# Kernel tuning notes

Hardware: AMD Instinct MI355X
Metric: run time of the kernel (lower is better)

The kernel has to match this reference:

```python
import jax, jax.numpy as jnp
import numpy as np

N, C, G = 50000, 30, 1000   # cells, classes, genes
E = 800000                   # edges
OUT = 8                      # GATv2 out channels, heads=1


def setup_inputs() -> dict:
    key = jax.random.key(0)
    ks = jax.random.split(key, 12)
    X = jax.random.normal(ks[0], (N, G), dtype=jnp.float32)
    Mu = jax.random.normal(ks[1], (C, G), dtype=jnp.float32)
    Var = jax.random.uniform(ks[2], (C, G), dtype=jnp.float32) + 0.5  # strictly positive
    edge_index = jax.random.randint(ks[3], (2, E), 0, N, dtype=jnp.int64)
    # learned params
    W = 0.01 * jax.random.normal(ks[4], (N, C), dtype=jnp.float32)   # torch init zeros; small noise for nontrivial P
    S = jnp.ones((N, 1), dtype=jnp.float32)
    sc = 1.0 / np.sqrt(G)
    Wl = sc * jax.random.normal(ks[5], (OUT, G), dtype=jnp.float32)  # lin_l weight
    bl = jnp.zeros((OUT,), dtype=jnp.float32)
    Wr = sc * jax.random.normal(ks[6], (OUT, G), dtype=jnp.float32)  # lin_r weight
    br = jnp.zeros((OUT,), dtype=jnp.float32)
    att = jax.random.normal(ks[7], (OUT,), dtype=jnp.float32) / np.sqrt(OUT)
    return {"X": X, "Mu": Mu, "Var": Var, "edge_index": edge_index,
            "W": W, "S": S, "Wl": Wl, "bl": bl, "Wr": Wr, "br": br, "att": att}


def reference(X, Mu, Var, edge_index, W, S, Wl, bl, Wr, br, att):
    n = X.shape[0]
    P = jax.nn.softmax(W, axis=1)                       # [N,C]
    # Gaussian log-likelihood term. Expand (X - Mu*S)^2/Var summed over genes:
    invVar = 1.0 / Var                                  # [C,G]
    A = (X * X) @ invVar.T                              # [N,C]  sum X^2/Var
    B = X @ (Mu * invVar).T                             # [N,C]  sum X*Mu/Var
    D = jnp.sum(Mu * Mu * invVar, axis=1)               # [C]    sum Mu^2/Var
    Fmat = -0.5 * (A - 2.0 * S * B + (S * S) * D[None, :])  # [N,C]
    ll_prot = jnp.sum(P * Fmat) / n

    # GATv2 attention (heads=1, add_self_loops=False)
    x_l = X @ Wl.T + bl                                 # [N,8] source transform
    x_r = X @ Wr.T + br                                 # [N,8] target transform
    src, dst = edge_index[0], edge_index[1]
    m = jax.nn.leaky_relu(x_l[src] + x_r[dst], negative_slope=0.2)  # [E,8]
    e = m @ att                                         # [E]
    # edge-softmax grouped by destination node
    emax = jax.ops.segment_max(e, dst, num_segments=n)  # [N]
    e_exp = jnp.exp(e - emax[dst])                      # [E]
    denom = jax.ops.segment_sum(e_exp, dst, num_segments=n)  # [N]
    alpha = e_exp / (denom[dst] + 1e-16)                # [E]

    ce_space = -jnp.sum(P[src] * alpha[:, None] * jnp.log(P[dst] + 1e-8)) / n
    return ll_prot, ce_space, P
```

## Files before the change

### kernel.cpp

```cpp
#include <hip/hip_runtime.h>
#include <math.h>

#define N_CELLS 50000
#define C_CLS   30
#define G_GENES 1000
#define E_EDGES 800000
#define KPAD    1024

typedef __attribute__((ext_vector_type(8))) short bf16x8;
typedef __attribute__((ext_vector_type(4))) float f32x4;

__device__ __forceinline__ unsigned f2bf_u(float f) {
    unsigned u = __float_as_uint(f);
    return (u + 0x7fffu + ((u >> 16) & 1u)) >> 16;
}
__device__ __forceinline__ unsigned pack2(float lo, float hi) {
    return f2bf_u(lo) | (f2bf_u(hi) << 16);
}

__device__ __forceinline__ float lrelu02(float v) { return v > 0.f ? v : 0.2f * v; }

__global__ void prep_kernel(const float* __restrict__ Mu, const float* __restrict__ Var,
                            const float* __restrict__ Wl, const float* __restrict__ Wr,
                            unsigned short* __restrict__ CoefB, float* __restrict__ Dvec) {
    const int r = blockIdx.x;
    const int t = threadIdx.x;
    __shared__ float red[256];
    float dacc = 0.f;
    for (int g = t; g < KPAD; g += 256) {
        float v = 0.f;
        if (g < G_GENES) {
            if (r < 30) {
                float iv = 1.0f / Var[r * G_GENES + g];
                float mu = Mu[r * G_GENES + g];
                v = iv;
                dacc += mu * mu * iv;
            } else if (r >= 32) {
                int i = r - 32;
                if (i < 30)      v = Mu[i * G_GENES + g] / Var[i * G_GENES + g];
                else if (i < 38) v = Wl[(i - 30) * G_GENES + g];
                else if (i < 46) v = Wr[(i - 38) * G_GENES + g];
            }
        }
        CoefB[r * KPAD + g] = (unsigned short)f2bf_u(v);
    }
    if (r < 30) {
        red[t] = dacc;
        __syncthreads();
        for (int s = 128; s > 0; s >>= 1) {
            if (t < s) red[t] += red[t + s];
            __syncthreads();
        }
        if (t == 0) Dvec[r] = red[0];
    }
}

__global__ __launch_bounds__(256) void main_rows_kernel(
    const float* __restrict__ X, const float* __restrict__ W,
    const float* __restrict__ S, const float* __restrict__ bl,
    const float* __restrict__ br, const unsigned short* __restrict__ CoefB,
    const float* __restrict__ Dvec,
    float* __restrict__ out,
    float* __restrict__ logP, float* __restrict__ xl, float* __restrict__ xr)
{
    __shared__ __align__(16) char smem[30720];
    unsigned short* Xt  = (unsigned short*)smem;
    unsigned short* X2t = (unsigned short*)(smem + 9216);
    unsigned short* Ct  = (unsigned short*)(smem + 18432);
    float* ob = (float*)smem;

    const int t    = threadIdx.x;
    const int w    = t >> 6;
    const int l    = t & 63;
    const int l15  = l & 15;
    const int quad = l >> 4;
    const int rowbase = blockIdx.x * 64;

    f32x4 acc[5];
#pragma unroll
    for (int i = 0; i < 5; i++) acc[i] = (f32x4){0.f, 0.f, 0.f, 0.f};

    const int srow = t >> 2;
    const int sq   = t & 3;
    const int n_g  = rowbase + srow;
    const bool rowok = (n_g < N_CELLS);
    const float* xrow = X + (size_t)n_g * G_GENES;

    for (int kt = 0; kt < KPAD; kt += 64) {
        __syncthreads();
        {
            const int kb = kt + sq * 16;
            float v[16];
#pragma unroll
            for (int i = 0; i < 4; i++) {
                int k = kb + i * 4;
                float4 f = make_float4(0.f, 0.f, 0.f, 0.f);
                if (rowok && k + 3 < G_GENES) f = *(const float4*)&xrow[k];
                v[i * 4 + 0] = f.x; v[i * 4 + 1] = f.y;
                v[i * 4 + 2] = f.z; v[i * 4 + 3] = f.w;
            }
            unsigned px[8], p2[8];
#pragma unroll
            for (int i = 0; i < 8; i++) {
                px[i] = pack2(v[2 * i], v[2 * i + 1]);
                p2[i] = pack2(v[2 * i] * v[2 * i], v[2 * i + 1] * v[2 * i + 1]);
            }
            int4* dx  = (int4*)&Xt [srow * 72 + sq * 16];
            int4* dx2 = (int4*)&X2t[srow * 72 + sq * 16];
            dx [0] = make_int4(px[0], px[1], px[2], px[3]);
            dx [1] = make_int4(px[4], px[5], px[6], px[7]);
            dx2[0] = make_int4(p2[0], p2[1], p2[2], p2[3]);
            dx2[1] = make_int4(p2[4], p2[5], p2[6], p2[7]);
        }
        for (int u = t; u < 640; u += 256) {
            int row = u >> 3;
            int kk  = (u & 7) * 8;
            *(int4*)&Ct[row * 72 + kk] = *(const int4*)&CoefB[row * KPAD + kt + kk];
        }
        __syncthreads();

#pragma unroll
        for (int ks = 0; ks < 2; ks++) {
            const int koff = ks * 32 + quad * 8;
            bf16x8 ax  = *(bf16x8*)&Xt [(w * 16 + l15) * 72 + koff];
            bf16x8 ax2 = *(bf16x8*)&X2t[(w * 16 + l15) * 72 + koff];
#pragma unroll
            for (int nt = 0; nt < 5; nt++) {
                bf16x8 b = *(bf16x8*)&Ct[(nt * 16 + l15) * 72 + koff];
                acc[nt] = __builtin_amdgcn_mfma_f32_16x16x32_bf16(
                    nt < 2 ? ax2 : ax, b, acc[nt], 0, 0, 0);
            }
        }
    }

    __syncthreads();
#pragma unroll
    for (int nt = 0; nt < 5; nt++)
#pragma unroll
        for (int r = 0; r < 4; r++)
            ob[(w * 16 + quad * 4 + r) * 81 + nt * 16 + l15] = acc[nt][r];
    __syncthreads();

    if (t < 64) {
        float llrow = 0.f;
        int n = rowbase + t;
        if (n < N_CELLS) {
            float wv[30];
            const float2* wrow = (const float2*)&W[(size_t)n * 30];
            float m = -1e30f;
#pragma unroll
            for (int c = 0; c < 15; c++) {
                float2 f = wrow[c];
                wv[2 * c] = f.x; wv[2 * c + 1] = f.y;
                m = fmaxf(m, fmaxf(f.x, f.y));
            }
            float s = 0.f;
#pragma unroll
            for (int c = 0; c < 30; c++) { wv[c] = expf(wv[c] - m); s += wv[c]; }
            float inv = 1.0f / s;
            float Sn  = S[n];
            float Sn2 = Sn * Sn;
#pragma unroll
            for (int c = 0; c < 30; c++) {
                float p = wv[c] * inv;
                out[2 + (size_t)n * 30 + c] = p;
                logP[(size_t)n * 30 + c] = logf(p + 1e-8f);
                float Av = ob[t * 81 + c];
                float Bv = ob[t * 81 + 32 + c];
                float F  = -0.5f * (Av - 2.0f * Sn * Bv + Sn2 * Dvec[c]);
                llrow += p * F;
            }
#pragma unroll
            for (int o = 0; o < 8; o++) {
                xl[(size_t)n * 8 + o] = ob[t * 81 + 62 + o] + bl[o];
                xr[(size_t)n * 8 + o] = ob[t * 81 + 70 + o] + br[o];
            }
        }
        for (int off = 32; off > 0; off >>= 1) llrow += __shfl_down(llrow, off, 64);
        if (t == 0) atomicAdd(&out[0], llrow * (1.0f / N_CELLS));
    }
}

__global__ void edge_passA(const int* __restrict__ ei, const float* __restrict__ xl,
                           const float* __restrict__ xr, const float* __restrict__ att,
                           float* __restrict__ evals, float* __restrict__ denom) {
    int e = blockIdx.x * 256 + threadIdx.x;
    if (e >= E_EDGES) return;
    int src = ei[e];
    int dst = ei[E_EDGES + e];
    const float4* lp = (const float4*)&xl[(size_t)src * 8];
    const float4* rp = (const float4*)&xr[(size_t)dst * 8];
    float4 l0 = lp[0], l1 = lp[1];
    float4 r0 = rp[0], r1 = rp[1];
    float ev = 0.f;
    ev += lrelu02(l0.x + r0.x) * att[0];
    ev += lrelu02(l0.y + r0.y) * att[1];
    ev += lrelu02(l0.z + r0.z) * att[2];
    ev += lrelu02(l0.w + r0.w) * att[3];
    ev += lrelu02(l1.x + r1.x) * att[4];
    ev += lrelu02(l1.y + r1.y) * att[5];
    ev += lrelu02(l1.z + r1.z) * att[6];
    ev += lrelu02(l1.w + r1.w) * att[7];
    float p = __expf(ev);
    evals[e] = p;
    atomicAdd(&denom[dst], p);
}

__global__ void edge_passB(const int* __restrict__ ei, const float* __restrict__ evals,
                           const float* __restrict__ denom,
                           const float* __restrict__ P, const float* __restrict__ logP,
                           float* __restrict__ out) {
    int e = blockIdx.x * 256 + threadIdx.x;
    float contrib = 0.f;
    if (e < E_EDGES) {
        int src = ei[e];
        int dst = ei[E_EDGES + e];
        float alpha = evals[e] / (denom[dst] + 1e-16f);
        const float2* ps = (const float2*)&P[(size_t)src * 30];
        const float2* ld = (const float2*)&logP[(size_t)dst * 30];
        float dot = 0.f;
#pragma unroll
        for (int c = 0; c < 15; c++) {
            float2 a = ps[c];
            float2 b = ld[c];
            dot += a.x * b.x + a.y * b.y;
        }
        contrib = -alpha * dot;
    }
    for (int off = 32; off > 0; off >>= 1) contrib += __shfl_down(contrib, off, 64);
    __shared__ float wsum[4];
    int lane = threadIdx.x & 63;
    int wid  = threadIdx.x >> 6;
    if (lane == 0) wsum[wid] = contrib;
    __syncthreads();
    if (threadIdx.x == 0) {
        float ssum = wsum[0] + wsum[1] + wsum[2] + wsum[3];
        atomicAdd(&out[1], ssum * (1.0f / N_CELLS));
    }
}

extern "C" void kernel_launch(void* const* d_in, const int* in_sizes, int n_in,
                              void* d_out, int out_size, void* d_ws, size_t ws_size,
                              hipStream_t stream) {
    const float* X   = (const float*)d_in[0];
    const float* Mu  = (const float*)d_in[1];
    const float* Var = (const float*)d_in[2];
    const int*   ei  = (const int*)d_in[3];
    const float* W   = (const float*)d_in[4];
    const float* S   = (const float*)d_in[5];
    const float* Wl  = (const float*)d_in[6];
    const float* bl  = (const float*)d_in[7];
    const float* Wr  = (const float*)d_in[8];
    const float* br  = (const float*)d_in[9];
    const float* att = (const float*)d_in[10];

    float* out = (float*)d_out;

    float* wsf   = (float*)d_ws;
    unsigned short* CoefB = (unsigned short*)wsf;
    float* Dvec  = wsf + 40960;
    float* logP  = wsf + 40992;
    float* xl    = wsf + 1540992;
    float* xr    = wsf + 1940992;
    float* evals = wsf + 2340992;
    float* denom = wsf + 3140992;

    hipMemsetAsync(out, 0, 2 * sizeof(float), stream);
    hipMemsetAsync(denom, 0, (size_t)N_CELLS * sizeof(float), stream);

    prep_kernel<<<80, 256, 0, stream>>>(Mu, Var, Wl, Wr, CoefB, Dvec);
    main_rows_kernel<<<(N_CELLS + 63) / 64, 256, 0, stream>>>(
        X, W, S, bl, br, CoefB, Dvec, out, logP, xl, xr);
    edge_passA<<<(E_EDGES + 255) / 256, 256, 0, stream>>>(ei, xl, xr, att, evals, denom);
    edge_passB<<<(E_EDGES + 255) / 256, 256, 0, stream>>>(ei, evals, denom, out + 2, logP, out);
}
```

Baseline: 461.3 us.

## Load MFMA operands directly from global, split edge dot across lanes, fold memsets

The GEMM kernel drops its LDS staging and barriers: each lane loads its own X row slice straight from global memory into MFMA A operands and reads the bf16 coefficient tile directly from global/L2. The edge cross-entropy pass now uses 8 lanes per edge, each loading a 4-class chunk, which coalesces P/logP reads better at the cost of 8x more threads. The two memsets are folded into the prep kernel to remove launches. Per-lane X loads are less coalesced (32B chunks per row, spread across 16 rows), so the GEMM's global access pattern may get worse.

```diff
diff --git a/kernel.cpp b/kernel.cpp
--- a/kernel.cpp
+++ b/kernel.cpp
@@ -22,7 +22,8 @@
 
 __global__ void prep_kernel(const float* __restrict__ Mu, const float* __restrict__ Var,
                             const float* __restrict__ Wl, const float* __restrict__ Wr,
-                            unsigned short* __restrict__ CoefB, float* __restrict__ Dvec) {
+                            unsigned short* __restrict__ CoefB, float* __restrict__ Dvec,
+                            float* __restrict__ denom, float* __restrict__ out) {
     const int r = blockIdx.x;
     const int t = threadIdx.x;
     __shared__ float red[256];
@@ -44,6 +45,9 @@
         }
         CoefB[r * KPAD + g] = (unsigned short)f2bf_u(v);
     }
+    for (int i = blockIdx.x * 256 + t; i < N_CELLS; i += 80 * 256) denom[i] = 0.f;
+    if (r == 31 && t < 2) out[t] = 0.f;
+
     if (r < 30) {
         red[t] = dacc;
         __syncthreads();
@@ -63,11 +67,7 @@
     float* __restrict__ out,
     float* __restrict__ logP, float* __restrict__ xl, float* __restrict__ xr)
 {
-    __shared__ __align__(16) char smem[30720];
-    unsigned short* Xt  = (unsigned short*)smem;
-    unsigned short* X2t = (unsigned short*)(smem + 9216);
-    unsigned short* Ct  = (unsigned short*)(smem + 18432);
-    float* ob = (float*)smem;
+    __shared__ float ob[64 * 81];
 
     const int t    = threadIdx.x;
     const int w    = t >> 6;
@@ -75,65 +75,40 @@
     const int l15  = l & 15;
     const int quad = l >> 4;
     const int rowbase = blockIdx.x * 64;
+    const int myrow = rowbase + w * 16 + l15;
+    const bool rowok = (myrow < N_CELLS);
+    const float* __restrict__ xrow = X + (size_t)myrow * G_GENES;
 
     f32x4 acc[5];
 #pragma unroll
     for (int i = 0; i < 5; i++) acc[i] = (f32x4){0.f, 0.f, 0.f, 0.f};
 
-    const int srow = t >> 2;
-    const int sq   = t & 3;
-    const int n_g  = rowbase + srow;
-    const bool rowok = (n_g < N_CELLS);
-    const float* xrow = X + (size_t)n_g * G_GENES;
-
-    for (int kt = 0; kt < KPAD; kt += 64) {
-        __syncthreads();
-        {
-            const int kb = kt + sq * 16;
-            float v[16];
-#pragma unroll
-            for (int i = 0; i < 4; i++) {
-                int k = kb + i * 4;
-                float4 f = make_float4(0.f, 0.f, 0.f, 0.f);
-                if (rowok && k + 3 < G_GENES) f = *(const float4*)&xrow[k];
-                v[i * 4 + 0] = f.x; v[i * 4 + 1] = f.y;
-                v[i * 4 + 2] = f.z; v[i * 4 + 3] = f.w;
-            }
-            unsigned px[8], p2[8];
-#pragma unroll
-            for (int i = 0; i < 8; i++) {
-                px[i] = pack2(v[2 * i], v[2 * i + 1]);
-                p2[i] = pack2(v[2 * i] * v[2 * i], v[2 * i + 1] * v[2 * i + 1]);
-            }
-            int4* dx  = (int4*)&Xt [srow * 72 + sq * 16];
-            int4* dx2 = (int4*)&X2t[srow * 72 + sq * 16];
-            dx [0] = make_int4(px[0], px[1], px[2], px[3]);
-            dx [1] = make_int4(px[4], px[5], px[6], px[7]);
-            dx2[0] = make_int4(p2[0], p2[1], p2[2], p2[3]);
-            dx2[1] = make_int4(p2[4], p2[5], p2[6], p2[7]);
-        }
-        for (int u = t; u < 640; u += 256) {
-            int row = u >> 3;
-            int kk  = (u & 7) * 8;
-            *(int4*)&Ct[row * 72 + kk] = *(const int4*)&CoefB[row * KPAD + kt + kk];
-        }
-        __syncthreads();
-
-#pragma unroll
-        for (int ks = 0; ks < 2; ks++) {
-            const int koff = ks * 32 + quad * 8;
-            bf16x8 ax  = *(bf16x8*)&Xt [(w * 16 + l15) * 72 + koff];
-            bf16x8 ax2 = *(bf16x8*)&X2t[(w * 16 + l15) * 72 + koff];
-#pragma unroll
-            for (int nt = 0; nt < 5; nt++) {
-                bf16x8 b = *(bf16x8*)&Ct[(nt * 16 + l15) * 72 + koff];
-                acc[nt] = __builtin_amdgcn_mfma_f32_16x16x32_bf16(
-                    nt < 2 ? ax2 : ax, b, acc[nt], 0, 0, 0);
-            }
-        }
-    }
-
-    __syncthreads();
+#pragma unroll 2
+    for (int kt = 0; kt < KPAD; kt += 32) {
+        const int k0 = kt + quad * 8;
+        float4 f0 = make_float4(0.f, 0.f, 0.f, 0.f);
+        float4 f1 = make_float4(0.f, 0.f, 0.f, 0.f);
+        if (rowok && k0 < G_GENES) {
+            f0 = *(const float4*)&xrow[k0];
+            f1 = *(const float4*)&xrow[k0 + 4];
+        }
+        union { unsigned u[4]; bf16x8 v; } ua, u2;
+        ua.u[0] = pack2(f0.x, f0.y);
+        ua.u[1] = pack2(f0.z, f0.w);
+        ua.u[2] = pack2(f1.x, f1.y);
+        ua.u[3] = pack2(f1.z, f1.w);
+        u2.u[0] = pack2(f0.x * f0.x, f0.y * f0.y);
+        u2.u[1] = pack2(f0.z * f0.z, f0.w * f0.w);
+        u2.u[2] = pack2(f1.x * f1.x, f1.y * f1.y);
+        u2.u[3] = pack2(f1.z * f1.z, f1.w * f1.w);
+#pragma unroll
+        for (int nt = 0; nt < 5; nt++) {
+            bf16x8 b = *(const bf16x8*)&CoefB[(nt * 16 + l15) * KPAD + k0];
+            acc[nt] = __builtin_amdgcn_mfma_f32_16x16x32_bf16(
+                nt < 2 ? u2.v : ua.v, b, acc[nt], 0, 0, 0);
+        }
+    }
+
 #pragma unroll
     for (int nt = 0; nt < 5; nt++)
 #pragma unroll
@@ -206,37 +181,44 @@
     atomicAdd(&denom[dst], p);
 }
 
-__global__ void edge_passB(const int* __restrict__ ei, const float* __restrict__ evals,
-                           const float* __restrict__ denom,
-                           const float* __restrict__ P, const float* __restrict__ logP,
-                           float* __restrict__ out) {
-    int e = blockIdx.x * 256 + threadIdx.x;
+__global__ __launch_bounds__(256) void edge_passB(
+    const int* __restrict__ ei, const float* __restrict__ evals,
+    const float* __restrict__ denom, const float* __restrict__ P,
+    const float* __restrict__ logP, float* __restrict__ out) {
+    const int t    = threadIdx.x;
+    const int lane = t & 63;
+    const int sub  = lane >> 3;
+    const int cl   = t & 7;
+    const long wid = (long)blockIdx.x * 4 + (t >> 6);
+    const long e   = wid * 8 + sub;
     float contrib = 0.f;
     if (e < E_EDGES) {
         int src = ei[e];
         int dst = ei[E_EDGES + e];
         float alpha = evals[e] / (denom[dst] + 1e-16f);
-        const float2* ps = (const float2*)&P[(size_t)src * 30];
-        const float2* ld = (const float2*)&logP[(size_t)dst * 30];
-        float dot = 0.f;
-#pragma unroll
-        for (int c = 0; c < 15; c++) {
-            float2 a = ps[c];
-            float2 b = ld[c];
-            dot += a.x * b.x + a.y * b.y;
+        int c0 = cl * 4;
+        const float* ps = &P[(size_t)src * 30 + c0];
+        const float* ld = &logP[(size_t)dst * 30 + c0];
+        float dot;
+        if (cl < 7) {
+            float2 p0 = *(const float2*)ps;
+            float2 p1 = *(const float2*)(ps + 2);
+            float2 q0 = *(const float2*)ld;
+            float2 q1 = *(const float2*)(ld + 2);
+            dot = p0.x * q0.x + p0.y * q0.y + p1.x * q1.x + p1.y * q1.y;
+        } else {
+            float2 p0 = *(const float2*)ps;
+            float2 q0 = *(const float2*)ld;
+            dot = p0.x * q0.x + p0.y * q0.y;
         }
         contrib = -alpha * dot;
     }
-    for (int off = 32; off > 0; off >>= 1) contrib += __shfl_down(contrib, off, 64);
+    for (int m = 1; m < 64; m <<= 1) contrib += __shfl_xor(contrib, m, 64);
     __shared__ float wsum[4];
-    int lane = threadIdx.x & 63;
-    int wid  = threadIdx.x >> 6;
-    if (lane == 0) wsum[wid] = contrib;
+    if (lane == 0) wsum[t >> 6] = contrib;
     __syncthreads();
-    if (threadIdx.x == 0) {
-        float ssum = wsum[0] + wsum[1] + wsum[2] + wsum[3];
-        atomicAdd(&out[1], ssum * (1.0f / N_CELLS));
-    }
+    if (t == 0)
+        atomicAdd(&out[1], (wsum[0] + wsum[1] + wsum[2] + wsum[3]) * (1.0f / N_CELLS));
 }
 
 extern "C" void kernel_launch(void* const* d_in, const int* in_sizes, int n_in,
@@ -265,12 +247,10 @@
     float* evals = wsf + 2340992;
     float* denom = wsf + 3140992;
 
-    hipMemsetAsync(out, 0, 2 * sizeof(float), stream);
-    hipMemsetAsync(denom, 0, (size_t)N_CELLS * sizeof(float), stream);
-
-    prep_kernel<<<80, 256, 0, stream>>>(Mu, Var, Wl, Wr, CoefB, Dvec);
+    prep_kernel<<<80, 256, 0, stream>>>(Mu, Var, Wl, Wr, CoefB, Dvec, denom, out);
     main_rows_kernel<<<(N_CELLS + 63) / 64, 256, 0, stream>>>(
         X, W, S, bl, br, CoefB, Dvec, out, logP, xl, xr);
     edge_passA<<<(E_EDGES + 255) / 256, 256, 0, stream>>>(ei, xl, xr, att, evals, denom);
-    edge_passB<<<(E_EDGES + 255) / 256, 256, 0, stream>>>(ei, evals, denom, out + 2, logP, out);
-}
+    edge_passB<<<(E_EDGES * 8 + 255) / 256, 256, 0, stream>>>(ei, evals, denom,
+                                                              out + 2, logP, out);
+}
```

Result: slower. 727.5 us (+57.7%).
